# Optimization experiments

Measured on AMD Instinct MI355X. Metric: run time of the kernel, lower is better.

Reference implementation:

```python
import jax, jax.numpy as jnp
import numpy as np

LAYERS = 10
EPS = 1e-08


def setup_inputs() -> dict:
    key = jax.random.key(0)
    # [B, agents, N, N] assignment logits; row 0 along dim 2 is the depot row
    output = jax.random.normal(key, (32, 8, 512, 512), dtype=jnp.float32)
    return {"output": output}


def reference(output):
    # Max-subtraction for numerical stability before exp.
    # Depot row: max over dim 3 only. Other rows: max over dims (1, 3).
    if LAYERS > 0:
        depots_max = jnp.max(output[:, :, :1, :], axis=3, keepdims=True)
        others_max = jnp.max(output[:, :, 1:, :], axis=(1, 3), keepdims=True)
        output = jnp.concatenate(
            [output[:, :, :1, :] - depots_max,
             output[:, :, 1:, :] - others_max],
            axis=2,
        )
    output = jnp.exp(output)
    # Sinkhorn-style alternating normalization; transpose(2,3) each iter
    # alternates which axis gets normalized.
    for _ in range(LAYERS):
        output = jnp.maximum(output, EPS)
        starts = output[:, :, :1, :]
        starts = starts / jnp.sum(starts, axis=3, keepdims=True)
        nexts = output[:, :, 1:, :]
        nexts = nexts / jnp.sum(nexts, axis=(1, 3), keepdims=True)
        output = jnp.concatenate([starts, nexts], axis=2)
        output = jnp.swapaxes(output, 2, 3)
    if LAYERS % 2 != 0:
        output = jnp.swapaxes(output, 2, 3)
    return output
```

## Files before the change

### kernel.cpp

```cpp
#include <hip/hip_runtime.h>
#include <hip/hip_cooperative_groups.h>
#include <math.h>

#define B 32
#define H 8
#define N 512
#define NBLK 256
#define TPB 512
#define RPB 64
#define OFF_PA   8388608
#define OFF_PB   (OFF_PA + 131072)
#define OFF_C0A  (OFF_PB + 131072)
#define OFF_C0B  (OFF_C0A + 2048)

typedef float f32x4 __attribute__((ext_vector_type(4)));

__device__ __forceinline__ float2 atomLoad2(const float* p) {
    unsigned long long u = __hip_atomic_load(
        reinterpret_cast<const unsigned long long*>(p),
        __ATOMIC_RELAXED, __HIP_MEMORY_SCOPE_AGENT);
    union { unsigned long long u; float2 f; } cvt; cvt.u = u;
    return cvt.f;
}
__device__ __forceinline__ void atomStore(float* p, float v) {
    __hip_atomic_store(p, v, __ATOMIC_RELAXED, __HIP_MEMORY_SCOPE_AGENT);
}

__device__ __forceinline__ void group_barrier(int* cnt, int target) {
    __syncthreads();
    if (threadIdx.x == 0) {
        __hip_atomic_fetch_add(cnt, 1, __ATOMIC_RELAXED, __HIP_MEMORY_SCOPE_AGENT);
        while (__hip_atomic_load(cnt, __ATOMIC_RELAXED, __HIP_MEMORY_SCOPE_AGENT) < target)
            __builtin_amdgcn_s_sleep(1);
    }
    __syncthreads();
}

__global__ void k_zero(int* __restrict__ counters) {
    counters[threadIdx.x] = 0;
}

__global__ __launch_bounds__(TPB) void k_coopb(const float* __restrict__ in,
                                               float* __restrict__ partA,
                                               float* __restrict__ partB,
                                               float* __restrict__ c0pA,
                                               float* __restrict__ c0pB,
                                               float* __restrict__ rv,
                                               float* __restrict__ r0v,
                                               float* __restrict__ cv,
                                               float* __restrict__ c0v,
                                               int* __restrict__ counters) {
    __shared__ float Gs[RPB][N];
    __shared__ float E0g[N];
    __shared__ float vec[N];
    __shared__ float EcS[H][RPB];
    __shared__ float rloc[RPB];
    __shared__ float c0rec[H];
    __shared__ float r0loc_s;

    const int blk = blockIdx.x;
    const int b = blk >> 3;
    const int g = blk & 7;
    const int rbase = g * RPB;
    const bool owner = (g == 0);
    const int tid = threadIdx.x;
    const int w = tid >> 6, lane = tid & 63;
    int* cnt = counters + b * 16;

    const int il4 = tid >> 7;
    const int j4 = tid & 127;
    const size_t inb = (size_t)b * H * N * N;
    for (int c = 0; c < 16; ++c) {
        const int il = c * 4 + il4;
        const float* rowbase = in + inb + (size_t)(rbase + il) * N + j4 * 4;
        float4 xv[8];
#pragma unroll
        for (int h = 0; h < H; ++h)
            xv[h] = *reinterpret_cast<const float4*>(rowbase + (size_t)h * N * N);
        float4 acc = make_float4(0.f, 0.f, 0.f, 0.f);
#pragma unroll
        for (int h = 0; h < H; ++h) {
            float4 e;
            e.x = __expf(xv[h].x); e.y = __expf(xv[h].y);
            e.z = __expf(xv[h].z); e.w = __expf(xv[h].w);
            acc.x += e.x; acc.y += e.y; acc.z += e.z; acc.w += e.w;
            if (j4 == 0) EcS[h][il] = e.x;
        }
        *reinterpret_cast<float4*>(&Gs[il][j4 * 4]) = acc;
    }
    if (tid < 128) {
        const float4 xr = *reinterpret_cast<const float4*>(in + inb + (size_t)g * N * N + tid * 4);
        E0g[tid * 4 + 0] = __expf(xr.x);
        E0g[tid * 4 + 1] = __expf(xr.y);
        E0g[tid * 4 + 2] = __expf(xr.z);
        E0g[tid * 4 + 3] = __expf(xr.w);
    }
    __syncthreads();
    const float E00g = E0g[0];

    for (int it = 0; it < 5; ++it) {
        if (it == 0) {
            vec[tid] = (tid == 0) ? 0.0f : 1.0f;
            if (tid < H) c0rec[tid] = 1.0f;
        } else {
            const float* pr = (it & 1) ? partB : partA;
            pr += ((size_t)b * N + tid) * 8;
            float cs = 0.0f;
#pragma unroll
            for (int k = 0; k < 4; ++k) {
                float2 d = atomLoad2(pr + 2 * k);
                cs += d.x + d.y;
            }
            vec[tid] = (tid == 0) ? 0.0f : 1.0f / cs;
            if (tid < H) {
                const float* qr = (it & 1) ? c0pB : c0pA;
                qr += (b * 8 + tid) * 8;
                float s = 0.0f;
#pragma unroll
                for (int k = 0; k < 4; ++k) {
                    float2 d = atomLoad2(qr + 2 * k);
                    s += d.x + d.y;
                }
                c0rec[tid] = 1.0f / s;
            }
        }
        __syncthreads();
        float cj[8];
#pragma unroll
        for (int k = 0; k < 8; ++k) cj[k] = vec[lane + 64 * k];
#pragma unroll
        for (int r8 = 0; r8 < 8; ++r8) {
            const int il = w * 8 + r8;
            float pacc = 0.0f;
#pragma unroll
            for (int k = 0; k < 8; ++k) pacc += Gs[il][lane + 64 * k] * cj[k];
#pragma unroll
            for (int s = 32; s > 0; s >>= 1) pacc += __shfl_down(pacc, s, 64);
            if (lane == 0) {
                float s2 = pacc;
#pragma unroll
                for (int h = 0; h < H; ++h) s2 += EcS[h][il] * c0rec[h];
                float rva = 1.0f / s2;
                rloc[il] = rva;
                if (it == 4) rv[b * N + rbase + il] = rva;
            }
        }
        if (w == g) {
            float pacc = 0.0f;
#pragma unroll
            for (int k = 0; k < 8; ++k) pacc += E0g[lane + 64 * k] * cj[k];
#pragma unroll
            for (int s = 32; s > 0; s >>= 1) pacc += __shfl_down(pacc, s, 64);
            if (lane == 0) {
                float v = 1.0f / (pacc + E00g * c0rec[g]);
                r0loc_s = v;
                if (it == 4) r0v[b * H + g] = v;
            }
        }
        __syncthreads();
        {
            float* pw = ((it + 1) & 1) ? partB : partA;
            float* qw = ((it + 1) & 1) ? c0pB : c0pA;
            const float r0l = r0loc_s;
            float acc2 = 0.0f;
            const int il0 = owner ? 1 : 0;
#pragma unroll 8
            for (int il = il0; il < RPB; ++il) acc2 += Gs[il][tid] * rloc[il];
            acc2 += E0g[tid] * r0l;
            atomStore(&pw[((size_t)b * N + tid) * 8 + g], acc2);
            float q = EcS[w][lane] * ((owner && lane == 0) ? 0.0f : rloc[lane]);
            if (w == g && lane == 0) q += E00g * r0l;
#pragma unroll
            for (int s = 32; s > 0; s >>= 1) q += __shfl_down(q, s, 64);
            if (lane == 0) atomStore(&qw[(b * 8 + w) * 8 + g], q);
        }
        group_barrier(cnt, (it + 1) * 8);
    }
    if (owner) {
        const float* pr = partB + ((size_t)b * N + tid) * 8;
        float cs = 0.0f;
#pragma unroll
        for (int k = 0; k < 4; ++k) {
            float2 d = atomLoad2(pr + 2 * k);
            cs += d.x + d.y;
        }
        cv[b * N + tid] = (tid == 0) ? 1.0f : 1.0f / cs;
        if (tid < H) {
            const float* qr = c0pB + (b * 8 + tid) * 8;
            float s = 0.0f;
#pragma unroll
            for (int k = 0; k < 4; ++k) {
                float2 d = atomLoad2(qr + 2 * k);
                s += d.x + d.y;
            }
            c0v[b * H + tid] = 1.0f / s;
        }
    }
}

__global__ __launch_bounds__(256) void k_final(const float* __restrict__ in,
                                               const float* __restrict__ rv,
                                               const float* __restrict__ r0v,
                                               const float* __restrict__ cv,
                                               const float* __restrict__ c0v,
                                               float* __restrict__ out) {
    const size_t v0 = (size_t)blockIdx.x * 2048 + threadIdx.x;
    float4 x[8];
#pragma unroll
    for (int s = 0; s < 8; ++s)
        x[s] = reinterpret_cast<const float4*>(in)[v0 + (size_t)s * 256];
#pragma unroll
    for (int s = 0; s < 8; ++s) {
        const size_t v = v0 + (size_t)s * 256;
        const int j4 = (int)(v & 127);
        size_t rest = v >> 7;
        const int i = (int)(rest & 511); rest >>= 9;
        const int h = (int)(rest & 7);
        const int b = (int)(rest >> 3);
        const float R = (i == 0) ? r0v[b * H + h] : rv[b * N + i];
        float4 cl = reinterpret_cast<const float4*>(cv + b * N)[j4];
        if (j4 == 0) cl.x = c0v[b * H + h];
        f32x4 o;
        o.x = __expf(x[s].x) * R * cl.x;
        o.y = __expf(x[s].y) * R * cl.y;
        o.z = __expf(x[s].z) * R * cl.z;
        o.w = __expf(x[s].w) * R * cl.w;
        __builtin_nontemporal_store(o, reinterpret_cast<f32x4*>(out) + v);
    }
}

extern "C" void kernel_launch(void* const* d_in, const int* in_sizes, int n_in,
                              void* d_out, int out_size, void* d_ws, size_t ws_size,
                              hipStream_t stream) {
    (void)in_sizes; (void)n_in; (void)out_size; (void)ws_size;
    const float* in = (const float*)d_in[0];
    float* out = (float*)d_out;
    float* ws = (float*)d_ws;

    float* rv  = ws;
    float* cv  = ws + 16384;
    float* r0v = ws + 32768;
    float* c0v = ws + 33024;
    int* counters = (int*)(ws + 33280);

    float* pA  = out + OFF_PA;
    float* pB  = out + OFF_PB;
    float* c0A = out + OFF_C0A;
    float* c0B = out + OFF_C0B;

    k_zero<<<1, 512, 0, stream>>>(counters);

    void* args[] = {(void*)&in, (void*)&pA, (void*)&pB, (void*)&c0A, (void*)&c0B,
                    (void*)&rv, (void*)&r0v, (void*)&cv, (void*)&c0v, (void*)&counters};
    hipLaunchCooperativeKernel(reinterpret_cast<void*>(k_coopb), dim3(NBLK), dim3(TPB),
                               args, 0, stream);

    k_final<<<8192, 256, 0, stream>>>(in, rv, r0v, cv, c0v, out);
}
```

Before: 182.5 us.

## Fuse final scaling pass into cooperative Sinkhorn kernel, dropping k_final launch

The separate k_final kernel is removed. Each cooperative block now writes the output for its own 64 rows across all heads, using row scales kept in shared memory and column scales that every block rebuilds from the partial sums. This saves a kernel launch, the global round trip of the rv/cv vectors, and spreads the final streaming pass over the cooperative grid. In exchange the 128 MB read and write now runs on only 256 blocks with heavy LDS use, which may lower memory-level parallelism compared with 8192 small blocks. Scratch buffers also move from the output tail into the workspace.

```diff
diff --git a/kernel.cpp b/kernel.cpp
--- a/kernel.cpp
+++ b/kernel.cpp
@@ -8,13 +8,12 @@
 #define NBLK 256
 #define TPB 512
 #define RPB 64
-#define OFF_PA   8388608
-#define OFF_PB   (OFF_PA + 131072)
-#define OFF_C0A  (OFF_PB + 131072)
-#define OFF_C0B  (OFF_C0A + 2048)
 
 typedef float f32x4 __attribute__((ext_vector_type(4)));
 
+__device__ __forceinline__ float atomLoad(const float* p) {
+    return __hip_atomic_load(p, __ATOMIC_RELAXED, __HIP_MEMORY_SCOPE_AGENT);
+}
 __device__ __forceinline__ float2 atomLoad2(const float* p) {
     unsigned long long u = __hip_atomic_load(
         reinterpret_cast<const unsigned long long*>(p),
@@ -41,14 +40,12 @@
 }
 
 __global__ __launch_bounds__(TPB) void k_coopb(const float* __restrict__ in,
+                                               float* __restrict__ out,
                                                float* __restrict__ partA,
                                                float* __restrict__ partB,
                                                float* __restrict__ c0pA,
                                                float* __restrict__ c0pB,
-                                               float* __restrict__ rv,
-                                               float* __restrict__ r0v,
-                                               float* __restrict__ cv,
-                                               float* __restrict__ c0v,
+                                               float* __restrict__ r0g,
                                                int* __restrict__ counters) {
     __shared__ float Gs[RPB][N];
     __shared__ float E0g[N];
@@ -56,6 +53,7 @@
     __shared__ float EcS[H][RPB];
     __shared__ float rloc[RPB];
     __shared__ float c0rec[H];
+    __shared__ float r0s[H];
     __shared__ float r0loc_s;
 
     const int blk = blockIdx.x;
@@ -140,9 +138,7 @@
                 float s2 = pacc;
 #pragma unroll
                 for (int h = 0; h < H; ++h) s2 += EcS[h][il] * c0rec[h];
-                float rva = 1.0f / s2;
-                rloc[il] = rva;
-                if (it == 4) rv[b * N + rbase + il] = rva;
+                rloc[il] = 1.0f / s2;
             }
         }
         if (w == g) {
@@ -154,7 +150,7 @@
             if (lane == 0) {
                 float v = 1.0f / (pacc + E00g * c0rec[g]);
                 r0loc_s = v;
-                if (it == 4) r0v[b * H + g] = v;
+                if (it == 4) atomStore(r0g + b * 8 + g, v);
             }
         }
         __syncthreads();
@@ -176,7 +172,8 @@
         }
         group_barrier(cnt, (it + 1) * 8);
     }
-    if (owner) {
+
+    {
         const float* pr = partB + ((size_t)b * N + tid) * 8;
         float cs = 0.0f;
 #pragma unroll
@@ -184,7 +181,7 @@
             float2 d = atomLoad2(pr + 2 * k);
             cs += d.x + d.y;
         }
-        cv[b * N + tid] = (tid == 0) ? 1.0f : 1.0f / cs;
+        vec[tid] = (tid == 0) ? 1.0f : 1.0f / cs;
         if (tid < H) {
             const float* qr = c0pB + (b * 8 + tid) * 8;
             float s = 0.0f;
@@ -193,39 +190,34 @@
                 float2 d = atomLoad2(qr + 2 * k);
                 s += d.x + d.y;
             }
-            c0v[b * H + tid] = 1.0f / s;
-        }
-    }
-}
-
-__global__ __launch_bounds__(256) void k_final(const float* __restrict__ in,
-                                               const float* __restrict__ rv,
-                                               const float* __restrict__ r0v,
-                                               const float* __restrict__ cv,
-                                               const float* __restrict__ c0v,
-                                               float* __restrict__ out) {
-    const size_t v0 = (size_t)blockIdx.x * 2048 + threadIdx.x;
-    float4 x[8];
-#pragma unroll
-    for (int s = 0; s < 8; ++s)
-        x[s] = reinterpret_cast<const float4*>(in)[v0 + (size_t)s * 256];
-#pragma unroll
-    for (int s = 0; s < 8; ++s) {
-        const size_t v = v0 + (size_t)s * 256;
-        const int j4 = (int)(v & 127);
-        size_t rest = v >> 7;
-        const int i = (int)(rest & 511); rest >>= 9;
-        const int h = (int)(rest & 7);
-        const int b = (int)(rest >> 3);
-        const float R = (i == 0) ? r0v[b * H + h] : rv[b * N + i];
-        float4 cl = reinterpret_cast<const float4*>(cv + b * N)[j4];
-        if (j4 == 0) cl.x = c0v[b * H + h];
-        f32x4 o;
-        o.x = __expf(x[s].x) * R * cl.x;
-        o.y = __expf(x[s].y) * R * cl.y;
-        o.z = __expf(x[s].z) * R * cl.z;
-        o.w = __expf(x[s].w) * R * cl.w;
-        __builtin_nontemporal_store(o, reinterpret_cast<f32x4*>(out) + v);
+            c0rec[tid] = 1.0f / s;
+            r0s[tid] = atomLoad(r0g + b * 8 + tid);
+        }
+    }
+    __syncthreads();
+
+    for (int c = 0; c < 16; ++c) {
+        const int il = c * 4 + il4;
+        const int gi = rbase + il;
+        const float rl = rloc[il];
+        const size_t rowoff = inb + (size_t)gi * N + j4 * 4;
+        const float4 c4 = *reinterpret_cast<const float4*>(&vec[j4 * 4]);
+        float4 xv[8];
+#pragma unroll
+        for (int h = 0; h < H; ++h)
+            xv[h] = *reinterpret_cast<const float4*>(in + rowoff + (size_t)h * N * N);
+#pragma unroll
+        for (int h = 0; h < H; ++h) {
+            const float R = (gi == 0) ? r0s[h] : rl;
+            const float cx = (j4 == 0) ? c0rec[h] : c4.x;
+            f32x4 o;
+            o.x = __expf(xv[h].x) * R * cx;
+            o.y = __expf(xv[h].y) * R * c4.y;
+            o.z = __expf(xv[h].z) * R * c4.z;
+            o.w = __expf(xv[h].w) * R * c4.w;
+            __builtin_nontemporal_store(
+                o, reinterpret_cast<f32x4*>(out + rowoff + (size_t)h * N * N));
+        }
     }
 }
 
@@ -237,23 +229,17 @@
     float* out = (float*)d_out;
     float* ws = (float*)d_ws;
 
-    float* rv  = ws;
-    float* cv  = ws + 16384;
-    float* r0v = ws + 32768;
-    float* c0v = ws + 33024;
-    int* counters = (int*)(ws + 33280);
-
-    float* pA  = out + OFF_PA;
-    float* pB  = out + OFF_PB;
-    float* c0A = out + OFF_C0A;
-    float* c0B = out + OFF_C0B;
+    int* counters = (int*)ws;
+    float* pA  = ws + 512;
+    float* pB  = pA + B * N * 8;
+    float* c0A = pB + B * N * 8;
+    float* c0B = c0A + B * 8 * 8;
+    float* r0g = c0B + B * 8 * 8;
 
     k_zero<<<1, 512, 0, stream>>>(counters);
 
-    void* args[] = {(void*)&in, (void*)&pA, (void*)&pB, (void*)&c0A, (void*)&c0B,
-                    (void*)&rv, (void*)&r0v, (void*)&cv, (void*)&c0v, (void*)&counters};
+    void* args[] = {(void*)&in, (void*)&out, (void*)&pA, (void*)&pB,
+                    (void*)&c0A, (void*)&c0B, (void*)&r0g, (void*)&counters};
     hipLaunchCooperativeKernel(reinterpret_cast<void*>(k_coopb), dim3(NBLK), dim3(TPB),
                                args, 0, stream);
-
-    k_final<<<8192, 256, 0, stream>>>(in, rv, r0v, cv, c0v, out);
-}
+}
```

Result: no change. 182.6 us (+0.0%).
